# Kernel optimization log

Measured on AMD Instinct MI355X. Metric: run time of the kernel, lower is better.

The kernel has to match this reference:

```python
import jax, jax.numpy as jnp
import numpy as np

N, F_IN, F_OUT = 8192, 256, 128


def setup_inputs() -> dict:
    key = jax.random.key(0)
    k1, k2, k3, k4 = jax.random.split(key, 4)
    h = jax.random.normal(k1, (N, F_IN), dtype=jnp.float32)
    adj = jax.random.randint(k2, (N, N), 0, 2, dtype=jnp.int32)
    # xavier-uniform-like init scales
    w_lim = float(np.sqrt(6.0 / (F_IN + F_OUT)))
    a_lim = float(np.sqrt(6.0 / (2 * F_OUT + 1)))
    W = jax.random.uniform(k3, (F_IN, F_OUT), jnp.float32, -w_lim, w_lim)
    a = jax.random.uniform(k4, (2 * F_OUT, 1), jnp.float32, -a_lim, a_lim)
    return {"h": h, "adj": adj, "W": W, "a": a}


def reference(h, adj, W, a):
    # Wh: [N, F_OUT]
    Wh = h @ W
    # Fused form of the pairwise-concat score: e[i,j] = leakyrelu(Wh_i.a1 + Wh_j.a2)
    a1 = a[:F_OUT]   # [F_OUT, 1]
    a2 = a[F_OUT:]   # [F_OUT, 1]
    s1 = Wh @ a1     # [N, 1]
    s2 = Wh @ a2     # [N, 1]
    e = jax.nn.leaky_relu(s1 + s2.T, negative_slope=0.2)  # [N, N]
    e = jnp.where(adj > 0, e, jnp.float32(-9e15))
    attention = jax.nn.softmax(e, axis=1)
    return attention @ Wh  # [N, F_OUT]
```

## Files before the change

### kernel.cpp

```cpp
#include <hip/hip_runtime.h>

#define N_   8192
#define FIN  256
#define FOUT 128
#define NW   (N_ / 32)

typedef _Float16 f16x8 __attribute__((ext_vector_type(8)));
typedef float    f32x4 __attribute__((ext_vector_type(4)));
typedef unsigned int uint;

#define LDS_BARRIER() asm volatile("s_waitcnt lgkmcnt(0)\n\ts_barrier" ::: "memory")

__global__ __launch_bounds__(256) void k_pack(
    const int* __restrict__ adj, uint* __restrict__ bm)
{
    const int wid = (blockIdx.x * 256 + threadIdx.x) >> 6;
    const int l   = threadIdx.x & 63;
    const int4* __restrict__ arow = (const int4*)(adj + (size_t)wid * N_);
    uint* __restrict__ brow = bm + (size_t)wid * NW;

    #pragma unroll 2
    for (int jb = 0; jb < 32; ++jb) {
        int4 av = arow[jb * 64 + l];
        uint nib = (uint)(av.x != 0) | ((uint)(av.y != 0) << 1)
                 | ((uint)(av.z != 0) << 2) | ((uint)(av.w != 0) << 3);
        uint v = nib | (__shfl_xor(nib, 1, 64) << 4);
        v = v | (__shfl_xor(v, 2, 64) << 8);
        v = v | (__shfl_xor(v, 4, 64) << 16);
        if ((l & 7) == 0)
            brow[jb * 8 + (l >> 3)] = v;
    }
}

__global__ __launch_bounds__(256) void k_wh(
    const float* __restrict__ h, const float* __restrict__ W,
    const float* __restrict__ a, float* __restrict__ Wh,
    float* __restrict__ s1, float* __restrict__ s2)
{
    __shared__ float hrow[2][FIN];
    __shared__ float rbuf[2][2][2];
    const int t   = threadIdx.x;
    const int rh  = t >> 7;
    const int c   = t & 127;
    const int row = (blockIdx.x << 1) + rh;

    hrow[rh][c]       = h[(size_t)row * FIN + c];
    hrow[rh][c + 128] = h[(size_t)row * FIN + c + 128];
    __syncthreads();

    float acc = 0.f;
    #pragma unroll 8
    for (int k = 0; k < FIN; ++k)
        acc = fmaf(hrow[rh][k], W[k * FOUT + c], acc);

    Wh[(size_t)row * FOUT + c] = acc;

    float p1 = acc * a[c];
    float p2 = acc * a[FOUT + c];
    #pragma unroll
    for (int off = 32; off; off >>= 1) {
        p1 += __shfl_down(p1, off, 64);
        p2 += __shfl_down(p2, off, 64);
    }
    if ((t & 63) == 0) { rbuf[rh][c >> 6][0] = p1; rbuf[rh][c >> 6][1] = p2; }
    __syncthreads();
    if (c == 0) {
        const float k2 = 1.44269504088896f;
        s1[row] = (rbuf[rh][0][0] + rbuf[rh][1][0]) * k2;
        s2[row] = (rbuf[rh][0][1] + rbuf[rh][1][1]) * k2;
    }
}

__global__ __launch_bounds__(256) void k_tr(
    const float* __restrict__ Wh, _Float16* __restrict__ WhT)
{
    __shared__ float tile[64][129];
    const int t = threadIdx.x;
    const int rbase = blockIdx.x * 64;

    #pragma unroll
    for (int q = 0; q < 8; ++q) {
        int i4 = q * 256 + t;
        int r  = i4 >> 5;
        int c4 = (i4 & 31) * 4;
        *(float4*)&tile[r][c4] = *(const float4*)&Wh[(size_t)(rbase + r) * FOUT + c4];
    }
    __syncthreads();

    const int c = t >> 1, half = t & 1;
    _Float16 buf[32];
    #pragma unroll
    for (int r = 0; r < 32; ++r) buf[r] = (_Float16)tile[32 * half + r][c];
    #pragma unroll
    for (int q = 0; q < 4; ++q)
        *(f16x8*)&WhT[(size_t)c * N_ + rbase + 32 * half + 8 * q] = *(f16x8*)&buf[8 * q];
}

__global__ __launch_bounds__(512, 4) void k_attn(
    const uint* __restrict__ bm, const _Float16* __restrict__ WhT,
    const float* __restrict__ s1g, const float* __restrict__ s2g,
    float* __restrict__ num_g, float* __restrict__ den_g)
{
    __shared__ _Float16 pA[2][32][136];
    __shared__ float s2s[2048];

    const int t  = threadIdx.x;
    const int w  = t >> 6;
    const int l  = t & 63;

    const int rb    = blockIdx.x & 255;
    const int sp    = blockIdx.x >> 8;
    const int rbase = rb * 32;
    const int jbase = sp * 2048;

    *(float4*)&s2s[t * 4] = *(const float4*)&s2g[jbase + t * 4];

    const int r  = t >> 4;
    const int g  = t & 15;
    const int j0 = g << 3;
    const int shift = (g & 3) * 8;
    const float s1r = s1g[rbase + r];
    const uint* __restrict__ brow =
        bm + (size_t)(rbase + r) * NW + sp * 64 + (g >> 2);

    const int ln15 = l & 15, lq = l >> 4;
    const _Float16* __restrict__ bptr =
        WhT + (size_t)(16 * w + ln15) * N_ + jbase + 8 * lq;

    f32x4 acc0 = {0.f, 0.f, 0.f, 0.f};
    f32x4 acc1 = {0.f, 0.f, 0.f, 0.f};
    float denp = 0.f;

    auto computeP = [&](uint mv, int tile, int buf) {
        const float bias = -5.77078016f;
        const uint byte = mv >> shift;
        const float* s2p = &s2s[tile * 128 + j0];
        float4 sA = *(const float4*)(s2p);
        float4 sB = *(const float4*)(s2p + 4);
        float m, e;
        f16x8 pv;
        m = s1r + sA.x; e = fmaxf(m, 0.2f * m); pv[0] = (_Float16)((byte & 1u)   ? __builtin_amdgcn_exp2f(e + bias) : 0.f);
        m = s1r + sA.y; e = fmaxf(m, 0.2f * m); pv[1] = (_Float16)((byte & 2u)   ? __builtin_amdgcn_exp2f(e + bias) : 0.f);
        m = s1r + sA.z; e = fmaxf(m, 0.2f * m); pv[2] = (_Float16)((byte & 4u)   ? __builtin_amdgcn_exp2f(e + bias) : 0.f);
        m = s1r + sA.w; e = fmaxf(m, 0.2f * m); pv[3] = (_Float16)((byte & 8u)   ? __builtin_amdgcn_exp2f(e + bias) : 0.f);
        m = s1r + sB.x; e = fmaxf(m, 0.2f * m); pv[4] = (_Float16)((byte & 16u)  ? __builtin_amdgcn_exp2f(e + bias) : 0.f);
        m = s1r + sB.y; e = fmaxf(m, 0.2f * m); pv[5] = (_Float16)((byte & 32u)  ? __builtin_amdgcn_exp2f(e + bias) : 0.f);
        m = s1r + sB.z; e = fmaxf(m, 0.2f * m); pv[6] = (_Float16)((byte & 64u)  ? __builtin_amdgcn_exp2f(e + bias) : 0.f);
        m = s1r + sB.w; e = fmaxf(m, 0.2f * m); pv[7] = (_Float16)((byte & 128u) ? __builtin_amdgcn_exp2f(e + bias) : 0.f);
        denp += (float)pv[0] + (float)pv[1] + (float)pv[2] + (float)pv[3]
              + (float)pv[4] + (float)pv[5] + (float)pv[6] + (float)pv[7];
        *(f16x8*)&pA[buf][r][j0] = pv;
    };

    auto mmaTile = [&](int buf, int jb) {
        f16x8 b0 = *(const f16x8*)(bptr + jb);
        f16x8 b1 = *(const f16x8*)(bptr + jb + 32);
        f16x8 b2 = *(const f16x8*)(bptr + jb + 64);
        f16x8 b3 = *(const f16x8*)(bptr + jb + 96);
        const _Float16* a0p = &pA[buf][ln15][8 * lq];
        const _Float16* a1p = &pA[buf][16 + ln15][8 * lq];
        acc0 = __builtin_amdgcn_mfma_f32_16x16x32_f16(*(const f16x8*)(a0p),      b0, acc0, 0, 0, 0);
        acc1 = __builtin_amdgcn_mfma_f32_16x16x32_f16(*(const f16x8*)(a1p),      b0, acc1, 0, 0, 0);
        acc0 = __builtin_amdgcn_mfma_f32_16x16x32_f16(*(const f16x8*)(a0p + 32), b1, acc0, 0, 0, 0);
        acc1 = __builtin_amdgcn_mfma_f32_16x16x32_f16(*(const f16x8*)(a1p + 32), b1, acc1, 0, 0, 0);
        acc0 = __builtin_amdgcn_mfma_f32_16x16x32_f16(*(const f16x8*)(a0p + 64), b2, acc0, 0, 0, 0);
        acc1 = __builtin_amdgcn_mfma_f32_16x16x32_f16(*(const f16x8*)(a1p + 64), b2, acc1, 0, 0, 0);
        acc0 = __builtin_amdgcn_mfma_f32_16x16x32_f16(*(const f16x8*)(a0p + 96), b3, acc0, 0, 0, 0);
        acc1 = __builtin_amdgcn_mfma_f32_16x16x32_f16(*(const f16x8*)(a1p + 96), b3, acc1, 0, 0, 0);
    };

    uint mv0 = brow[0];
    uint mv1 = brow[4];

    LDS_BARRIER();
    computeP(mv0, 0, 0);
    LDS_BARRIER();

    for (int tt = 0; tt < 14; tt += 2) {
        {
            mv0 = brow[(tt + 2) * 4];
            mmaTile(0, tt * 128);
            computeP(mv1, tt + 1, 1);
            LDS_BARRIER();
        }
        {
            mv1 = brow[(tt + 3) * 4];
            mmaTile(1, (tt + 1) * 128);
            computeP(mv0, tt + 2, 0);
            LDS_BARRIER();
        }
    }
    mmaTile(0, 14 * 128);
    computeP(mv1, 15, 1);
    LDS_BARRIER();
    mmaTile(1, 15 * 128);

    denp += __shfl_xor(denp, 1, 64);
    denp += __shfl_xor(denp, 2, 64);
    denp += __shfl_xor(denp, 4, 64);
    denp += __shfl_xor(denp, 8, 64);
    if ((t & 15) == 0)
        den_g[(size_t)sp * N_ + rbase + r] = denp;

    const int colg = 16 * w + ln15;
    const int rq   = lq * 4;
    #pragma unroll
    for (int q = 0; q < 4; ++q) {
        num_g[((size_t)sp * N_ + rbase + rq + q)      * FOUT + colg] = acc0[q];
        num_g[((size_t)sp * N_ + rbase + 16 + rq + q) * FOUT + colg] = acc1[q];
    }
}

__global__ __launch_bounds__(256) void k_norm(
    const float* __restrict__ num_g, const float* __restrict__ den_g,
    float* __restrict__ out)
{
    const int idx4 = blockIdx.x * 256 + threadIdx.x;
    const int i  = idx4 >> 5;
    const int c4 = (idx4 & 31) * 4;

    float4 s = {0.f, 0.f, 0.f, 0.f};
    float  d = 0.f;
    #pragma unroll
    for (int sp = 0; sp < 4; ++sp) {
        float4 v = *(const float4*)(num_g + ((size_t)sp * N_ + i) * FOUT + c4);
        s.x += v.x; s.y += v.y; s.z += v.z; s.w += v.w;
        d += den_g[(size_t)sp * N_ + i];
    }
    const float inv = 1.f / d;
    float4 o = {s.x * inv, s.y * inv, s.z * inv, s.w * inv};
    *(float4*)&out[(size_t)i * FOUT + c4] = o;
}

extern "C" void kernel_launch(void* const* d_in, const int* in_sizes, int n_in,
                              void* d_out, int out_size, void* d_ws, size_t ws_size,
                              hipStream_t stream) {
    const float* h   = (const float*)d_in[0];
    const int*   adj = (const int*)d_in[1];
    const float* W   = (const float*)d_in[2];
    const float* a   = (const float*)d_in[3];
    float* out = (float*)d_out;

    char* ws = (char*)d_ws;
    float*    Wh  = (float*)ws;
    _Float16* WhT = (_Float16*)(ws + (4u << 20));
    float*    s1  = (float*)(ws + (6u << 20));
    float*    s2  = (float*)(ws + (6u << 20) + 32768);
    float*    num = (float*)(ws + (7u << 20));
    float*    den = (float*)(ws + (23u << 20));
    uint*     bmk = (uint*)(ws + (24u << 20));

    k_pack<<<2048,   256, 0, stream>>>(adj, bmk);
    k_wh  <<<N_ / 2, 256, 0, stream>>>(h, W, a, Wh, s1, s2);
    k_tr  <<<N_ / 64, 256, 0, stream>>>(Wh, WhT);
    k_attn<<<1024,  512, 0, stream>>>(bmk, WhT, s1, s2, num, den);
    k_norm<<<1024,  256, 0, stream>>>(num, den, out);
}
```

Measured before the change: 162.7 us.

## Retile attention kernel to 16-row blocks with swizzled LDS and interleaved MFMA

Shrinks each attention block from 32 rows and 512 threads to 16 rows and 256 threads, doubling the grid. Each wave now covers 32 output columns instead of 16, so every P fragment read from LDS feeds two MFMAs. The P tile drops its padding in favour of an XOR swizzle to avoid bank conflicts. The next tile's softmax-weight computation is interleaved with the current MFMA burst, which is raised with s_setprio. The trade-off is twice as many WhT global loads per row processed and more registers held per thread.

```diff
diff --git a/kernel.cpp b/kernel.cpp
--- a/kernel.cpp
+++ b/kernel.cpp
@@ -96,24 +96,25 @@
         *(f16x8*)&WhT[(size_t)c * N_ + rbase + 32 * half + 8 * q] = *(f16x8*)&buf[8 * q];
 }
 
-__global__ __launch_bounds__(512, 4) void k_attn(
+__global__ __launch_bounds__(256, 5) void k_attn(
     const uint* __restrict__ bm, const _Float16* __restrict__ WhT,
     const float* __restrict__ s1g, const float* __restrict__ s2g,
     float* __restrict__ num_g, float* __restrict__ den_g)
 {
-    __shared__ _Float16 pA[2][32][136];
+    __shared__ _Float16 pP[2][16][128];
     __shared__ float s2s[2048];
 
     const int t  = threadIdx.x;
     const int w  = t >> 6;
     const int l  = t & 63;
 
-    const int rb    = blockIdx.x & 255;
-    const int sp    = blockIdx.x >> 8;
-    const int rbase = rb * 32;
+    const int rb    = blockIdx.x & 511;
+    const int sp    = blockIdx.x >> 9;
+    const int rbase = rb * 16;
     const int jbase = sp * 2048;
 
-    *(float4*)&s2s[t * 4] = *(const float4*)&s2g[jbase + t * 4];
+    *(float4*)&s2s[t * 8]     = *(const float4*)&s2g[jbase + t * 8];
+    *(float4*)&s2s[t * 8 + 4] = *(const float4*)&s2g[jbase + t * 8 + 4];
 
     const int r  = t >> 4;
     const int g  = t & 15;
@@ -122,16 +123,18 @@
     const float s1r = s1g[rbase + r];
     const uint* __restrict__ brow =
         bm + (size_t)(rbase + r) * NW + sp * 64 + (g >> 2);
+    _Float16* const wp = &pP[0][0][0] + r * 128 + 8 * (g ^ (r & 7));
 
     const int ln15 = l & 15, lq = l >> 4;
-    const _Float16* __restrict__ bptr =
-        WhT + (size_t)(16 * w + ln15) * N_ + jbase + 8 * lq;
+    const _Float16* __restrict__ bp =
+        WhT + (size_t)(32 * w + ln15) * N_ + jbase + 8 * lq;
+    const _Float16* const ap = &pP[0][0][0] + ln15 * 128;
 
     f32x4 acc0 = {0.f, 0.f, 0.f, 0.f};
     f32x4 acc1 = {0.f, 0.f, 0.f, 0.f};
     float denp = 0.f;
 
-    auto computeP = [&](uint mv, int tile, int buf) {
+    auto computeP = [&](uint mv, int tile, int bufO) {
         const float bias = -5.77078016f;
         const uint byte = mv >> shift;
         const float* s2p = &s2s[tile * 128 + j0];
@@ -149,51 +152,82 @@
         m = s1r + sB.w; e = fmaxf(m, 0.2f * m); pv[7] = (_Float16)((byte & 128u) ? __builtin_amdgcn_exp2f(e + bias) : 0.f);
         denp += (float)pv[0] + (float)pv[1] + (float)pv[2] + (float)pv[3]
               + (float)pv[4] + (float)pv[5] + (float)pv[6] + (float)pv[7];
-        *(f16x8*)&pA[buf][r][j0] = pv;
+        *(f16x8*)(wp + bufO) = pv;
     };
 
-    auto mmaTile = [&](int buf, int jb) {
-        f16x8 b0 = *(const f16x8*)(bptr + jb);
-        f16x8 b1 = *(const f16x8*)(bptr + jb + 32);
-        f16x8 b2 = *(const f16x8*)(bptr + jb + 64);
-        f16x8 b3 = *(const f16x8*)(bptr + jb + 96);
-        const _Float16* a0p = &pA[buf][ln15][8 * lq];
-        const _Float16* a1p = &pA[buf][16 + ln15][8 * lq];
-        acc0 = __builtin_amdgcn_mfma_f32_16x16x32_f16(*(const f16x8*)(a0p),      b0, acc0, 0, 0, 0);
-        acc1 = __builtin_amdgcn_mfma_f32_16x16x32_f16(*(const f16x8*)(a1p),      b0, acc1, 0, 0, 0);
-        acc0 = __builtin_amdgcn_mfma_f32_16x16x32_f16(*(const f16x8*)(a0p + 32), b1, acc0, 0, 0, 0);
-        acc1 = __builtin_amdgcn_mfma_f32_16x16x32_f16(*(const f16x8*)(a1p + 32), b1, acc1, 0, 0, 0);
-        acc0 = __builtin_amdgcn_mfma_f32_16x16x32_f16(*(const f16x8*)(a0p + 64), b2, acc0, 0, 0, 0);
-        acc1 = __builtin_amdgcn_mfma_f32_16x16x32_f16(*(const f16x8*)(a1p + 64), b2, acc1, 0, 0, 0);
-        acc0 = __builtin_amdgcn_mfma_f32_16x16x32_f16(*(const f16x8*)(a0p + 96), b3, acc0, 0, 0, 0);
-        acc1 = __builtin_amdgcn_mfma_f32_16x16x32_f16(*(const f16x8*)(a1p + 96), b3, acc1, 0, 0, 0);
+    auto tileStep = [&](int bufR, int jb, uint mvN, int tileN, int bufW) {
+        const _Float16* bjb = bp + jb;
+        f16x8 b00 = *(const f16x8*)(bjb);
+        f16x8 b01 = *(const f16x8*)(bjb + 32);
+        f16x8 b02 = *(const f16x8*)(bjb + 64);
+        f16x8 b03 = *(const f16x8*)(bjb + 96);
+        f16x8 b10 = *(const f16x8*)(bjb + 16 * N_);
+        f16x8 b11 = *(const f16x8*)(bjb + 16 * N_ + 32);
+        f16x8 b12 = *(const f16x8*)(bjb + 16 * N_ + 64);
+        f16x8 b13 = *(const f16x8*)(bjb + 16 * N_ + 96);
+
+        const _Float16* ab = ap + bufR * 2048;
+        const int sw = (ln15 & 7);
+        f16x8 a0 = *(const f16x8*)(ab + 8 * ((0 + lq) ^ sw));
+        f16x8 a1 = *(const f16x8*)(ab + 8 * ((4 + lq) ^ sw));
+        f16x8 a2 = *(const f16x8*)(ab + 8 * ((8 + lq) ^ sw));
+        f16x8 a3 = *(const f16x8*)(ab + 8 * ((12 + lq) ^ sw));
+
+        computeP(mvN, tileN, bufW * 2048);
+
+        __builtin_amdgcn_s_setprio(1);
+        acc0 = __builtin_amdgcn_mfma_f32_16x16x32_f16(a0, b00, acc0, 0, 0, 0);
+        acc1 = __builtin_amdgcn_mfma_f32_16x16x32_f16(a0, b10, acc1, 0, 0, 0);
+        acc0 = __builtin_amdgcn_mfma_f32_16x16x32_f16(a1, b01, acc0, 0, 0, 0);
+        acc1 = __builtin_amdgcn_mfma_f32_16x16x32_f16(a1, b11, acc1, 0, 0, 0);
+        acc0 = __builtin_amdgcn_mfma_f32_16x16x32_f16(a2, b02, acc0, 0, 0, 0);
+        acc1 = __builtin_amdgcn_mfma_f32_16x16x32_f16(a2, b12, acc1, 0, 0, 0);
+        acc0 = __builtin_amdgcn_mfma_f32_16x16x32_f16(a3, b03, acc0, 0, 0, 0);
+        acc1 = __builtin_amdgcn_mfma_f32_16x16x32_f16(a3, b13, acc1, 0, 0, 0);
+        __builtin_amdgcn_s_setprio(0);
     };
 
     uint mv0 = brow[0];
     uint mv1 = brow[4];
-
     LDS_BARRIER();
     computeP(mv0, 0, 0);
     LDS_BARRIER();
 
     for (int tt = 0; tt < 14; tt += 2) {
-        {
-            mv0 = brow[(tt + 2) * 4];
-            mmaTile(0, tt * 128);
-            computeP(mv1, tt + 1, 1);
-            LDS_BARRIER();
-        }
-        {
-            mv1 = brow[(tt + 3) * 4];
-            mmaTile(1, (tt + 1) * 128);
-            computeP(mv0, tt + 2, 0);
-            LDS_BARRIER();
-        }
-    }
-    mmaTile(0, 14 * 128);
-    computeP(mv1, 15, 1);
+        mv0 = brow[(tt + 2) * 4];
+        tileStep(0, tt * 128, mv1, tt + 1, 1);
+        LDS_BARRIER();
+        mv1 = brow[(tt + 3) * 4];
+        tileStep(1, (tt + 1) * 128, mv0, tt + 2, 0);
+        LDS_BARRIER();
+    }
+    tileStep(0, 14 * 128, mv1, 15, 1);
     LDS_BARRIER();
-    mmaTile(1, 15 * 128);
+    {
+        const _Float16* bjb = bp + 15 * 128;
+        f16x8 b00 = *(const f16x8*)(bjb);
+        f16x8 b01 = *(const f16x8*)(bjb + 32);
+        f16x8 b02 = *(const f16x8*)(bjb + 64);
+        f16x8 b03 = *(const f16x8*)(bjb + 96);
+        f16x8 b10 = *(const f16x8*)(bjb + 16 * N_);
+        f16x8 b11 = *(const f16x8*)(bjb + 16 * N_ + 32);
+        f16x8 b12 = *(const f16x8*)(bjb + 16 * N_ + 64);
+        f16x8 b13 = *(const f16x8*)(bjb + 16 * N_ + 96);
+        const _Float16* ab = ap + 2048;
+        const int sw = (ln15 & 7);
+        f16x8 a0 = *(const f16x8*)(ab + 8 * ((0 + lq) ^ sw));
+        f16x8 a1 = *(const f16x8*)(ab + 8 * ((4 + lq) ^ sw));
+        f16x8 a2 = *(const f16x8*)(ab + 8 * ((8 + lq) ^ sw));
+        f16x8 a3 = *(const f16x8*)(ab + 8 * ((12 + lq) ^ sw));
+        acc0 = __builtin_amdgcn_mfma_f32_16x16x32_f16(a0, b00, acc0, 0, 0, 0);
+        acc1 = __builtin_amdgcn_mfma_f32_16x16x32_f16(a0, b10, acc1, 0, 0, 0);
+        acc0 = __builtin_amdgcn_mfma_f32_16x16x32_f16(a1, b01, acc0, 0, 0, 0);
+        acc1 = __builtin_amdgcn_mfma_f32_16x16x32_f16(a1, b11, acc1, 0, 0, 0);
+        acc0 = __builtin_amdgcn_mfma_f32_16x16x32_f16(a2, b02, acc0, 0, 0, 0);
+        acc1 = __builtin_amdgcn_mfma_f32_16x16x32_f16(a2, b12, acc1, 0, 0, 0);
+        acc0 = __builtin_amdgcn_mfma_f32_16x16x32_f16(a3, b03, acc0, 0, 0, 0);
+        acc1 = __builtin_amdgcn_mfma_f32_16x16x32_f16(a3, b13, acc1, 0, 0, 0);
+    }
 
     denp += __shfl_xor(denp, 1, 64);
     denp += __shfl_xor(denp, 2, 64);
@@ -202,12 +236,11 @@
     if ((t & 15) == 0)
         den_g[(size_t)sp * N_ + rbase + r] = denp;
 
-    const int colg = 16 * w + ln15;
-    const int rq   = lq * 4;
+    const int c0 = 32 * w + ln15;
     #pragma unroll
     for (int q = 0; q < 4; ++q) {
-        num_g[((size_t)sp * N_ + rbase + rq + q)      * FOUT + colg] = acc0[q];
-        num_g[((size_t)sp * N_ + rbase + 16 + rq + q) * FOUT + colg] = acc1[q];
+        num_g[((size_t)sp * N_ + rbase + 4 * lq + q) * FOUT + c0]      = acc0[q];
+        num_g[((size_t)sp * N_ + rbase + 4 * lq + q) * FOUT + c0 + 16] = acc1[q];
     }
 }
 
@@ -253,6 +286,6 @@
     k_pack<<<2048,   256, 0, stream>>>(adj, bmk);
     k_wh  <<<N_ / 2, 256, 0, stream>>>(h, W, a, Wh, s1, s2);
     k_tr  <<<N_ / 64, 256, 0, stream>>>(Wh, WhT);
-    k_attn<<<1024,  512, 0, stream>>>(bmk, WhT, s1, s2, num, den);
+    k_attn<<<2048,  256, 0, stream>>>(bmk, WhT, s1, s2, num, den);
     k_norm<<<1024,  256, 0, stream>>>(num, den, out);
 }
```

Result: slower. 214.4 us (+31.8%).
